# Optimization experiments

Measured on AMD Instinct MI355X. Metric: run time of the kernel, lower is better.

The kernel has to match this reference:

```python
import jax, jax.numpy as jnp
import numpy as np

CROWN_ROOT_W = 2.0
SMOOTH_W = 1.5
EXPECTED_RATIO = 1.2  # 'molars' ratio used for all classes in the original code


def setup_inputs() -> dict:
    key = jax.random.key(0)
    segmentation = jax.random.uniform(key, (2, 32, 64, 128, 128), dtype=jnp.float32)
    return {"segmentation": segmentation}


def reference(segmentation):
    # segmentation: [B, C, D, H, W]
    B, C, D, H, W = segmentation.shape

    # --- crown/root ratio loss (vectorized over the B*C python double loop) ---
    total = segmentation.sum(axis=(2, 3, 4))                       # [B, C]
    crown = segmentation[:, :, : D // 2].sum(axis=(2, 3, 4))       # [B, C]
    root = segmentation[:, :, D // 2 :].sum(axis=(2, 3, 4))        # [B, C]
    valid = (total > 0) & (root > 0)                               # branch conditions
    safe_root = jnp.where(root > 0, root, jnp.ones_like(root))
    ratio_loss = jnp.where(valid, (crown / safe_root - EXPECTED_RATIO) ** 2, 0.0)
    cr_loss = ratio_loss.sum() / (B * C)

    # --- 3D total-variation smoothness ---
    grad_x = jnp.abs(segmentation[:, :, :, :, 1:] - segmentation[:, :, :, :, :-1]).mean()
    grad_y = jnp.abs(segmentation[:, :, :, 1:, :] - segmentation[:, :, :, :-1, :]).mean()
    grad_z = jnp.abs(segmentation[:, :, 1:, :, :] - segmentation[:, :, :-1, :, :]).mean()
    tv_loss = grad_x + grad_y + grad_z

    crown_root = cr_loss * CROWN_ROOT_W
    smoothness = tv_loss * SMOOTH_W
    total_anatomy = crown_root + smoothness
    # dict in torch -> stacked [crown_root, smoothness, total_anatomy]
    return jnp.stack([crown_root, smoothness, total_anatomy])
```

## Files before the change

### kernel.cpp

```cpp
#include <hip/hip_runtime.h>

#define DD 64
#define HH 128
#define WW 128
#define BC 64
#define HALF_D 32
#define NBINS 32

#define WS_DOUBLES 224

__global__ __launch_bounds__(256) void anatomy_main(const float* __restrict__ seg,
                                                    double* __restrict__ ws) {
    const int w4      = threadIdx.x & 31;
    const int h_local = threadIdx.x >> 5;
    const int htile   = blockIdx.x;
    const int bc      = blockIdx.y;
    const int h       = htile * 8 + h_local;

    float crown = 0.f, root = 0.f, gx = 0.f, gy = 0.f, gz = 0.f;
    float4 prev = make_float4(0.f, 0.f, 0.f, 0.f);

    const size_t bcBase = (size_t)bc * DD * HH * WW;

    for (int d = 0; d < DD; ++d) {
        const float* row = seg + bcBase + ((size_t)d * HH + h) * WW;
        float4 v = ((const float4*)row)[w4];

        float s = v.x + v.y + v.z + v.w;
        if (d < HALF_D) crown += s; else root += s;

        gx += fabsf(v.y - v.x) + fabsf(v.z - v.y) + fabsf(v.w - v.z);
        float nx = __shfl_down(v.x, 1);
        if (w4 < 31) gx += fabsf(nx - v.w);

        if (h + 1 < HH) {
            float4 n = ((const float4*)(row + WW))[w4];
            gy += fabsf(n.x - v.x) + fabsf(n.y - v.y) + fabsf(n.z - v.z) + fabsf(n.w - v.w);
        }

        if (d > 0) {
            gz += fabsf(v.x - prev.x) + fabsf(v.y - prev.y) +
                  fabsf(v.z - prev.z) + fabsf(v.w - prev.w);
        }
        prev = v;
    }

    #pragma unroll
    for (int o = 32; o; o >>= 1) {
        crown += __shfl_down(crown, o);
        root  += __shfl_down(root,  o);
        gx    += __shfl_down(gx,    o);
        gy    += __shfl_down(gy,    o);
        gz    += __shfl_down(gz,    o);
    }

    __shared__ float red[4][5];
    const int wave = threadIdx.x >> 6;
    const int lane = threadIdx.x & 63;
    if (lane == 0) {
        red[wave][0] = crown; red[wave][1] = root;
        red[wave][2] = gx;    red[wave][3] = gy; red[wave][4] = gz;
    }
    __syncthreads();
    if (threadIdx.x == 0) {
        float c = 0.f, r = 0.f, x = 0.f, y = 0.f, z = 0.f;
        #pragma unroll
        for (int i = 0; i < 4; ++i) {
            c += red[i][0]; r += red[i][1];
            x += red[i][2]; y += red[i][3]; z += red[i][4];
        }
        const int bin = (int)((blockIdx.y * gridDim.x + blockIdx.x) & (NBINS - 1));
        atomicAdd(&ws[bc],            (double)c);
        atomicAdd(&ws[64 + bc],       (double)r);
        atomicAdd(&ws[128 + bin],     (double)x);
        atomicAdd(&ws[160 + bin],     (double)y);
        atomicAdd(&ws[192 + bin],     (double)z);
    }
}

__global__ void anatomy_finalize(const double* __restrict__ ws, float* __restrict__ out) {
    const int t = threadIdx.x;

    double crown = ws[t];
    double root  = ws[64 + t];
    double total = crown + root;
    double rl = 0.0;
    if (total > 0.0 && root > 0.0) {
        double r = crown / root - 1.2;
        rl = r * r;
    }
    double gx = (t < NBINS) ? ws[128 + t] : 0.0;
    double gy = (t < NBINS) ? ws[160 + t] : 0.0;
    double gz = (t < NBINS) ? ws[192 + t] : 0.0;

    #pragma unroll
    for (int o = 32; o; o >>= 1) {
        rl += __shfl_down(rl, o);
        gx += __shfl_down(gx, o);
        gy += __shfl_down(gy, o);
        gz += __shfl_down(gz, o);
    }

    if (t == 0) {
        const double n_gx = (double)BC * DD * HH * (WW - 1);
        const double n_gy = (double)BC * DD * (HH - 1) * WW;
        const double n_gz = (double)BC * (DD - 1) * HH * WW;
        double cr_loss    = (rl / (double)BC) * 2.0;
        double tv         = gx / n_gx + gy / n_gy + gz / n_gz;
        double smooth     = tv * 1.5;
        out[0] = (float)cr_loss;
        out[1] = (float)smooth;
        out[2] = (float)(cr_loss + smooth);
    }
}

extern "C" void kernel_launch(void* const* d_in, const int* in_sizes, int n_in,
                              void* d_out, int out_size, void* d_ws, size_t ws_size,
                              hipStream_t stream) {
    const float* seg = (const float*)d_in[0];
    float* out = (float*)d_out;
    double* ws = (double*)d_ws;

    hipMemsetAsync(d_ws, 0, WS_DOUBLES * sizeof(double), stream);

    dim3 grid(16, 64);
    anatomy_main<<<grid, 256, 0, stream>>>(seg, ws);
    anatomy_finalize<<<1, 64, 0, stream>>>(ws, out);
}
```

Measured before the change: 372.9 us.

## Replace atomics and memset with per-block partial writes and tree finalize

```diff
diff --git a/kernel.cpp b/kernel.cpp
--- a/kernel.cpp
+++ b/kernel.cpp
@@ -5,12 +5,11 @@
 #define WW 128
 #define BC 64
 #define HALF_D 32
-#define NBINS 32
+#define NBLK 1024
 
-#define WS_DOUBLES 224
 
 __global__ __launch_bounds__(256) void anatomy_main(const float* __restrict__ seg,
-                                                    double* __restrict__ ws) {
+                                                    float* __restrict__ ws) {
     const int w4      = threadIdx.x & 31;
     const int h_local = threadIdx.x >> 5;
     const int htile   = blockIdx.x;
@@ -18,13 +17,16 @@
     const int h       = htile * 8 + h_local;
 
     float crown = 0.f, root = 0.f, gx = 0.f, gy = 0.f, gz = 0.f;
+
+    const float* p  = seg + (size_t)bc * DD * HH * WW + (size_t)h * WW + w4 * 4;
+    const int nOff = (h == HH - 1) ? 0 : WW;
+
     float4 prev = make_float4(0.f, 0.f, 0.f, 0.f);
 
-    const size_t bcBase = (size_t)bc * DD * HH * WW;
-
     for (int d = 0; d < DD; ++d) {
-        const float* row = seg + bcBase + ((size_t)d * HH + h) * WW;
-        float4 v = ((const float4*)row)[w4];
+        float4 v = *(const float4*)p;
+        float4 n = *(const float4*)(p + nOff);
+        p += HH * WW;
 
         float s = v.x + v.y + v.z + v.w;
         if (d < HALF_D) crown += s; else root += s;
@@ -33,10 +35,7 @@
         float nx = __shfl_down(v.x, 1);
         if (w4 < 31) gx += fabsf(nx - v.w);
 
-        if (h + 1 < HH) {
-            float4 n = ((const float4*)(row + WW))[w4];
-            gy += fabsf(n.x - v.x) + fabsf(n.y - v.y) + fabsf(n.z - v.z) + fabsf(n.w - v.w);
-        }
+        gy += fabsf(n.x - v.x) + fabsf(n.y - v.y) + fabsf(n.z - v.z) + fabsf(n.w - v.w);
 
         if (d > 0) {
             gz += fabsf(v.x - prev.x) + fabsf(v.y - prev.y) +
@@ -69,29 +68,41 @@
             c += red[i][0]; r += red[i][1];
             x += red[i][2]; y += red[i][3]; z += red[i][4];
         }
-        const int bin = (int)((blockIdx.y * gridDim.x + blockIdx.x) & (NBINS - 1));
-        atomicAdd(&ws[bc],            (double)c);
-        atomicAdd(&ws[64 + bc],       (double)r);
-        atomicAdd(&ws[128 + bin],     (double)x);
-        atomicAdd(&ws[160 + bin],     (double)y);
-        atomicAdd(&ws[192 + bin],     (double)z);
+        const int slot = bc * 16 + htile;
+        ws[0 * NBLK + slot] = c;
+        ws[1 * NBLK + slot] = r;
+        ws[2 * NBLK + slot] = x;
+        ws[3 * NBLK + slot] = y;
+        ws[4 * NBLK + slot] = z;
     }
 }
 
-__global__ void anatomy_finalize(const double* __restrict__ ws, float* __restrict__ out) {
+__global__ __launch_bounds__(256) void anatomy_finalize(const float* __restrict__ ws,
+                                                        float* __restrict__ out) {
     const int t = threadIdx.x;
 
-    double crown = ws[t];
-    double root  = ws[64 + t];
-    double total = crown + root;
     double rl = 0.0;
-    if (total > 0.0 && root > 0.0) {
-        double r = crown / root - 1.2;
-        rl = r * r;
+    if (t < BC) {
+        double crown = 0.0, root = 0.0;
+        #pragma unroll
+        for (int i = 0; i < 16; ++i) {
+            crown += (double)ws[0 * NBLK + t * 16 + i];
+            root  += (double)ws[1 * NBLK + t * 16 + i];
+        }
+        double total = crown + root;
+        if (total > 0.0 && root > 0.0) {
+            double r = crown / root - 1.2;
+            rl = r * r;
+        }
     }
-    double gx = (t < NBINS) ? ws[128 + t] : 0.0;
-    double gy = (t < NBINS) ? ws[160 + t] : 0.0;
-    double gz = (t < NBINS) ? ws[192 + t] : 0.0;
+
+    double gx = 0.0, gy = 0.0, gz = 0.0;
+    #pragma unroll
+    for (int i = 0; i < 4; ++i) {
+        gx += (double)ws[2 * NBLK + t * 4 + i];
+        gy += (double)ws[3 * NBLK + t * 4 + i];
+        gz += (double)ws[4 * NBLK + t * 4 + i];
+    }
 
     #pragma unroll
     for (int o = 32; o; o >>= 1) {
@@ -101,13 +112,23 @@
         gz += __shfl_down(gz, o);
     }
 
+    __shared__ double red[4][4];
+    const int wave = t >> 6;
+    if ((t & 63) == 0) {
+        red[wave][0] = rl; red[wave][1] = gx; red[wave][2] = gy; red[wave][3] = gz;
+    }
+    __syncthreads();
     if (t == 0) {
+        double RL = 0, GX = 0, GY = 0, GZ = 0;
+        #pragma unroll
+        for (int i = 0; i < 4; ++i) {
+            RL += red[i][0]; GX += red[i][1]; GY += red[i][2]; GZ += red[i][3];
+        }
         const double n_gx = (double)BC * DD * HH * (WW - 1);
         const double n_gy = (double)BC * DD * (HH - 1) * WW;
         const double n_gz = (double)BC * (DD - 1) * HH * WW;
-        double cr_loss    = (rl / (double)BC) * 2.0;
-        double tv         = gx / n_gx + gy / n_gy + gz / n_gz;
-        double smooth     = tv * 1.5;
+        double cr_loss = (RL / (double)BC) * 2.0;
+        double smooth  = (GX / n_gx + GY / n_gy + GZ / n_gz) * 1.5;
         out[0] = (float)cr_loss;
         out[1] = (float)smooth;
         out[2] = (float)(cr_loss + smooth);
@@ -119,11 +140,9 @@
                               hipStream_t stream) {
     const float* seg = (const float*)d_in[0];
     float* out = (float*)d_out;
-    double* ws = (double*)d_ws;
-
-    hipMemsetAsync(d_ws, 0, WS_DOUBLES * sizeof(double), stream);
+    float* ws  = (float*)d_ws;
 
     dim3 grid(16, 64);
     anatomy_main<<<grid, 256, 0, stream>>>(seg, ws);
-    anatomy_finalize<<<1, 64, 0, stream>>>(ws, out);
+    anatomy_finalize<<<1, 256, 0, stream>>>(ws, out);
 }
```

Result: faster. 356.0 us (-4.5%).
